# Kernel optimization log

Hardware: AMD Instinct MI355X
Metric: run time of the kernel (lower is better)

Reference implementation:

```python
import jax, jax.numpy as jnp
import numpy as np

NUM_HEADS = 8

def setup_inputs() -> dict:
    key = jax.random.key(0)
    ks = jax.random.split(key, 9)
    b, s, d = 2, 2048, 512
    e = d * NUM_HEADS  # 4096
    sc = 0.02
    return {
        "x": jax.random.normal(ks[0], (b, s, d), jnp.float32),
        "Wq": jax.random.normal(ks[1], (e, d), jnp.float32) * sc,
        "bq": jax.random.normal(ks[2], (e,), jnp.float32) * sc,
        "Wk": jax.random.normal(ks[3], (e, d), jnp.float32) * sc,
        "bk": jax.random.normal(ks[4], (e,), jnp.float32) * sc,
        "Wv": jax.random.normal(ks[5], (e, d), jnp.float32) * sc,
        "bv": jax.random.normal(ks[6], (e,), jnp.float32) * sc,
        "Wo": jax.random.normal(ks[7], (d, e), jnp.float32) * sc,
        "bo": jax.random.normal(ks[8], (d,), jnp.float32) * sc,
    }

def reference(x, Wq, bq, Wk, bk, Wv, bv, Wo, bo):
    b, s, d = x.shape
    h = NUM_HEADS
    hd = d  # head_dim == model_dimension in this module
    # QKV projections: [b, s, h*hd]
    q = (x @ Wq.T + bq).reshape(b, s, h, hd)
    k = (x @ Wk.T + bk).reshape(b, s, h, hd)
    v = (x @ Wv.T + bv).reshape(b, s, h, hd)
    # scores: [b, h, s_q, s_k]
    scores = jnp.einsum("bqhd,bkhd->bhqk", q, k) / jnp.sqrt(jnp.float32(hd))
    attn = jax.nn.softmax(scores, axis=-1)
    ctx = jnp.einsum("bhqk,bkhd->bqhd", attn, v).reshape(b, s, h * hd)
    return ctx @ Wo.T + bo
```

## Files before the change

kernel.cpp:

```cpp
#include <hip/hip_runtime.h>
#include <hip/hip_bf16.h>

typedef __hip_bfloat16 bf16t;
typedef short bf16x8 __attribute__((ext_vector_type(8)));
typedef float f32x4 __attribute__((ext_vector_type(4)));

__device__ __forceinline__ float b2f(short s) {
    unsigned u = ((unsigned)(unsigned short)s) << 16;
    float f;
    __builtin_memcpy(&f, &u, 4);
    return f;
}

__device__ __forceinline__ unsigned short f2b(float f) {
    unsigned u;
    __builtin_memcpy(&u, &f, 4);
    unsigned r = (u + 0x7fffu + ((u >> 16) & 1u)) >> 16;
    return (unsigned short)r;
}

__device__ __forceinline__ void gload_lds16(const void* g, void* l) {
    __builtin_amdgcn_global_load_lds(
        (const __attribute__((address_space(1))) void*)g,
        (__attribute__((address_space(3))) void*)l,
        16, 0, 0);
}

template<int EPI>
__global__ __launch_bounds__(512, 2)
void gemm8p(const bf16t* __restrict__ Ag, const bf16t* __restrict__ Bg,
            void* __restrict__ Cg, const float* __restrict__ bias,
            int K, int lda, int ldb, int ldc,
            long aOffB, long aOffH, long bOffB, long bOffH,
            long cOffB, long cOffH, float scale)
{
    __shared__ __align__(16) char lds8[131072];

    unsigned gx = gridDim.x, gy = gridDim.y;
    unsigned nwg = gx * gy * gridDim.z;
    unsigned wg = (blockIdx.z * gy + blockIdx.y) * gx + blockIdx.x;
    if ((nwg & 7u) == 0u) wg = (wg & 7u) * (nwg >> 3) + (wg >> 3);
    const unsigned pz = wg / (gx * gy);
    const unsigned prem = wg - pz * gx * gy;
    const unsigned py = prem / gx;
    const unsigned px = prem - py * gx;

    const int zb = pz >> 3, zh = pz & 7;
    const int brow = py * 256;
    const int bcol = px * 256;

    const size_t ldab = (size_t)lda * 2;
    const size_t ldbb = (size_t)ldb * 2;
    const char* Agb = (const char*)(Ag + (size_t)zb * aOffB + (size_t)zh * aOffH)
                      + (size_t)brow * ldab;
    const char* Bgb = (const char*)(Bg + (size_t)zb * bOffB + (size_t)zh * bOffH)
                      + (size_t)bcol * ldbb;

    const int t    = threadIdx.x;
    const int lane = t & 63;
    const int wid  = t >> 6;
    const int wm   = wid >> 2;
    const int wn   = wid & 3;
    const int lr   = lane & 15;
    const int lk   = lane >> 4;

    const int srow = t >> 2;
    const int scg  = (t & 3) ^ ((srow >> 1) & 3);
    const size_t aSrc = (size_t)srow * ldab + (size_t)scg * 16;
    const size_t bSrc = (size_t)srow * ldbb + (size_t)scg * 16;
    const int dst0 = t * 16;
    char* ldsA = lds8;
    char* ldsB = lds8 + 65536;

    const int rchunk = lk ^ ((lr >> 1) & 3);
    const int aByte = (wm * 128 + lr) * 64 + rchunk * 16;
    const int bByte = (wn * 64 + lr) * 64 + rchunk * 16;

    f32x4 acc[8][4];
#pragma unroll
    for (int i = 0; i < 8; ++i)
#pragma unroll
        for (int j = 0; j < 4; ++j)
            acc[i][j] = (f32x4){0.f, 0.f, 0.f, 0.f};

    const int nk = K >> 5;

#define STAGE_A(kt, bufi) do {                                              \
        const char* s_ = Agb + (size_t)(kt) * 64 + aSrc;                    \
        char* d_ = ldsA + (bufi) * 16384 + dst0;                            \
        gload_lds16(s_, d_);                                                \
        gload_lds16(s_ + 128 * ldab, d_ + 8192);                            \
    } while (0)
#define STAGE_B(kt, bufi) do {                                              \
        const char* s_ = Bgb + (size_t)(kt) * 64 + bSrc;                    \
        char* d_ = ldsB + (bufi) * 16384 + dst0;                            \
        gload_lds16(s_, d_);                                                \
        gload_lds16(s_ + 128 * ldbb, d_ + 8192);                            \
    } while (0)

    const int npro = nk < 3 ? nk : 3;
    for (int p = 0; p < npro; ++p) { STAGE_A(p, p & 3); STAGE_B(p, p & 3); }
    if (npro == 3) asm volatile("s_waitcnt vmcnt(8)" ::: "memory");
    else           asm volatile("s_waitcnt vmcnt(0)" ::: "memory");
    __builtin_amdgcn_s_barrier();

    for (int kt = 0; kt < nk; ++kt) {
        const int buf  = kt & 3;
        const int bufS = (kt + 3) & 3;
        const bool st  = (kt + 3) < nk;
        const char* lA = ldsA + buf * 16384;
        const char* lB = ldsB + buf * 16384;

        bf16x8 af[4], bfv[4];
#pragma unroll
        for (int i = 0; i < 4; ++i) af[i]  = *(const bf16x8*)(lA + aByte + i * 1024);
#pragma unroll
        for (int j = 0; j < 4; ++j) bfv[j] = *(const bf16x8*)(lB + bByte + j * 1024);
        if (st) STAGE_A(kt + 3, bufS);
        __builtin_amdgcn_s_barrier();
        asm volatile("s_waitcnt lgkmcnt(0)" ::: "memory");
        __builtin_amdgcn_s_setprio(1);
#pragma unroll
        for (int i = 0; i < 4; ++i)
#pragma unroll
            for (int j = 0; j < 4; ++j)
                acc[i][j] = __builtin_amdgcn_mfma_f32_16x16x32_bf16(af[i], bfv[j], acc[i][j], 0, 0, 0);
        __builtin_amdgcn_s_setprio(0);
        __builtin_amdgcn_s_barrier();

        bf16x8 af2[4];
#pragma unroll
        for (int i = 0; i < 4; ++i) af2[i] = *(const bf16x8*)(lA + aByte + (i + 4) * 1024);
        if (st) STAGE_B(kt + 3, bufS);
        if (st)                  asm volatile("s_waitcnt vmcnt(8)" ::: "memory");
        else if (kt + 2 < nk)    asm volatile("s_waitcnt vmcnt(4)" ::: "memory");
        else if (kt + 1 < nk)    asm volatile("s_waitcnt vmcnt(0)" ::: "memory");
        __builtin_amdgcn_s_barrier();
        asm volatile("s_waitcnt lgkmcnt(0)" ::: "memory");
        __builtin_amdgcn_s_setprio(1);
#pragma unroll
        for (int i = 0; i < 4; ++i)
#pragma unroll
            for (int j = 0; j < 4; ++j)
                acc[i + 4][j] = __builtin_amdgcn_mfma_f32_16x16x32_bf16(af2[i], bfv[j], acc[i + 4][j], 0, 0, 0);
        __builtin_amdgcn_s_setprio(0);
        __builtin_amdgcn_s_barrier();
    }
#undef STAGE_A
#undef STAGE_B

    if (EPI == 0) {
        __syncthreads();
        unsigned short* lC = (unsigned short*)lds8;
#pragma unroll
        for (int i = 0; i < 8; ++i)
#pragma unroll
            for (int j = 0; j < 4; ++j) {
                int col = wn * 64 + j * 16 + lr;
                float badd = bias ? bias[bcol + col] : 0.f;
#pragma unroll
                for (int r = 0; r < 4; ++r) {
                    int row = wm * 128 + i * 16 + lk * 4 + r;
                    lC[row * 256 + col] = f2b(acc[i][j][r] * scale + badd);
                }
            }
        __syncthreads();
        unsigned short* C = (unsigned short*)((bf16t*)Cg + (size_t)zb * cOffB + (size_t)zh * cOffH);
#pragma unroll
        for (int p = 0; p < 16; ++p) {
            int c  = p * 512 + t;
            int row = c >> 5;
            int cc  = c & 31;
            bf16x8 v = *(const bf16x8*)(lC + (size_t)c * 8);
            *(bf16x8*)(C + (size_t)(brow + row) * ldc + bcol + cc * 8) = v;
        }
    } else {
        unsigned short* C = (unsigned short*)Cg;
#pragma unroll
        for (int i = 0; i < 8; ++i)
#pragma unroll
            for (int j = 0; j < 4; ++j) {
                int col = bcol + wn * 64 + j * 16 + lr;
                int hh = col >> 9, dd = col & 511;
                float badd = bias ? bias[col] : 0.f;
                int row0 = brow + wm * 128 + i * 16 + lk * 4;
                int bb = row0 >> 11, ss0 = row0 & 2047;
                ushort4 pack;
                pack.x = f2b(acc[i][j][0] * scale + badd);
                pack.y = f2b(acc[i][j][1] * scale + badd);
                pack.z = f2b(acc[i][j][2] * scale + badd);
                pack.w = f2b(acc[i][j][3] * scale + badd);
                size_t addr = ((((size_t)(bb * 8 + hh)) * 512 + dd) << 11) + (size_t)ss0;
                *(ushort4*)(C + addr) = pack;
            }
    }
}

__global__ __launch_bounds__(256)
void gemm_of32(const bf16t* __restrict__ Ag, const bf16t* __restrict__ Bg,
               float* __restrict__ Cg, const float* __restrict__ bias,
               int K, int lda, int ldb, int ldc)
{
    __shared__ __align__(16) bf16t As[128 * 32];
    __shared__ __align__(16) bf16t Bs[64 * 32];

    unsigned gx = gridDim.x, gy = gridDim.y;
    unsigned nwg = gx * gy;
    unsigned wg = blockIdx.y * gx + blockIdx.x;
    if ((nwg & 7u) == 0u) wg = (wg & 7u) * (nwg >> 3) + (wg >> 3);
    const unsigned py = wg / gx;
    const unsigned px = wg - py * gx;
    const int brow = py * 128;
    const int bcol = px * 64;

    const int t    = threadIdx.x;
    const int lane = t & 63;
    const int wid  = t >> 6;
    const int wr   = wid >> 1, wc = wid & 1;
    const int lr   = lane & 15;
    const int lk   = lane >> 4;

    const size_t ldab = (size_t)lda * 2;
    const size_t ldbb = (size_t)ldb * 2;

    f32x4 acc[4][2];
#pragma unroll
    for (int i = 0; i < 4; ++i)
#pragma unroll
        for (int j = 0; j < 2; ++j)
            acc[i][j] = (f32x4){0.f, 0.f, 0.f, 0.f};

    const int srow = t >> 2;
    const int scg  = (t & 3) ^ ((srow >> 1) & 3);
    const char* Abase = (const char*)Ag + (size_t)brow * ldab;
    const char* Bbase = (const char*)Bg + (size_t)bcol * ldbb;
    const size_t aSrc = (size_t)srow * ldab + (size_t)scg * 16;
    const size_t bSrc = (size_t)srow * ldbb + (size_t)scg * 16;
    char* AsB = (char*)As;
    char* BsB = (char*)Bs;

    const int rchunk = lk ^ ((lr >> 1) & 3);
    const int aByte = (wr * 64 + lr) * 64 + rchunk * 16;
    const int bByte = (wc * 32 + lr) * 64 + rchunk * 16;

    const int nk = K >> 5;
    for (int kt = 0; kt < nk; ++kt) {
        const size_t kOff = (size_t)kt * 64;
        gload_lds16(Abase + aSrc + kOff,             AsB + t * 16);
        gload_lds16(Abase + aSrc + 64 * ldab + kOff, AsB + t * 16 + 4096);
        gload_lds16(Bbase + bSrc + kOff,             BsB + t * 16);
        asm volatile("s_waitcnt vmcnt(0)" ::: "memory");
        __syncthreads();

        bf16x8 af[4], bfv[2];
#pragma unroll
        for (int i = 0; i < 4; ++i)
            af[i] = *(const bf16x8*)(AsB + aByte + i * 1024);
#pragma unroll
        for (int j = 0; j < 2; ++j)
            bfv[j] = *(const bf16x8*)(BsB + bByte + j * 1024);
#pragma unroll
        for (int i = 0; i < 4; ++i)
#pragma unroll
            for (int j = 0; j < 2; ++j)
                acc[i][j] = __builtin_amdgcn_mfma_f32_16x16x32_bf16(af[i], bfv[j], acc[i][j], 0, 0, 0);
        __syncthreads();
    }

    const int orow = brow + wr * 64;
    const int ocol = bcol + wc * 32;
#pragma unroll
    for (int i = 0; i < 4; ++i)
#pragma unroll
        for (int j = 0; j < 2; ++j) {
            int col = ocol + j * 16 + lr;
            float badd = bias[col];
#pragma unroll
            for (int r = 0; r < 4; ++r) {
                int row = orow + i * 16 + lk * 4 + r;
                Cg[(size_t)row * ldc + col] = acc[i][j][r] + badd;
            }
        }
}

__global__ __launch_bounds__(256)
void softmax2048(bf16t* __restrict__ Sp)
{
    size_t row = blockIdx.x;
    bf16x8* p = (bf16x8*)(Sp + row * 2048);
    int t = threadIdx.x;
    bf16x8 raw = p[t];
    float v[8];
    float mx = -3.0e38f;
#pragma unroll
    for (int i = 0; i < 8; ++i) { v[i] = b2f(raw[i]); mx = fmaxf(mx, v[i]); }
#pragma unroll
    for (int off = 1; off < 64; off <<= 1) mx = fmaxf(mx, __shfl_xor(mx, off));
    __shared__ float redm[4], reds[4];
    int wid = t >> 6, lane = t & 63;
    if (lane == 0) redm[wid] = mx;
    __syncthreads();
    mx = fmaxf(fmaxf(redm[0], redm[1]), fmaxf(redm[2], redm[3]));
    float sum = 0.f;
#pragma unroll
    for (int i = 0; i < 8; ++i) { v[i] = __expf(v[i] - mx); sum += v[i]; }
#pragma unroll
    for (int off = 1; off < 64; off <<= 1) sum += __shfl_xor(sum, off);
    if (lane == 0) reds[wid] = sum;
    __syncthreads();
    sum = reds[0] + reds[1] + reds[2] + reds[3];
    float inv = 1.0f / sum;
    bf16x8 o;
#pragma unroll
    for (int i = 0; i < 8; ++i) o[i] = (short)f2b(v[i] * inv);
    p[t] = o;
}

__global__ __launch_bounds__(256)
void cvt5(const float* __restrict__ s0, const float* __restrict__ s1,
          const float* __restrict__ s2, const float* __restrict__ s3,
          const float* __restrict__ s4,
          bf16t* __restrict__ d0, bf16t* __restrict__ d1,
          bf16t* __restrict__ d2, bf16t* __restrict__ d3,
          bf16t* __restrict__ d4)
{
    const float* s;
    bf16t* d;
    switch (blockIdx.y) {
        case 0: s = s0; d = d0; break;
        case 1: s = s1; d = d1; break;
        case 2: s = s2; d = d2; break;
        case 3: s = s3; d = d3; break;
        default: s = s4; d = d4; break;
    }
    int i = blockIdx.x * 256 + threadIdx.x;
    float4 f = ((const float4*)s)[i];
    ushort4 o;
    o.x = f2b(f.x); o.y = f2b(f.y); o.z = f2b(f.z); o.w = f2b(f.w);
    ((ushort4*)d)[i] = o;
}

extern "C" void kernel_launch(void* const* d_in, const int* in_sizes, int n_in,
                              void* d_out, int out_size, void* d_ws, size_t ws_size,
                              hipStream_t stream)
{
    const float* x  = (const float*)d_in[0];
    const float* Wq = (const float*)d_in[1];
    const float* bq = (const float*)d_in[2];
    const float* Wk = (const float*)d_in[3];
    const float* bk = (const float*)d_in[4];
    const float* Wv = (const float*)d_in[5];
    const float* bv = (const float*)d_in[6];
    const float* Wo = (const float*)d_in[7];
    const float* bo = (const float*)d_in[8];

    const int Bn = 2, Sn = 2048, Dn = 512, Hn = 8, En = 4096;
    const int Mn = Bn * Sn;
    const float scl = 0.044194173824159216f;

    bf16t* base = (bf16t*)d_ws;
    size_t off = 0;
    bf16t* Qb  = base + off; off += (size_t)Mn * En;
    bf16t* Kb  = base + off; off += (size_t)Mn * En;
    bf16t* Vt  = base + off; off += (size_t)Mn * En;
    bf16t* Xb  = base + off; off += (size_t)Mn * Dn;
    bf16t* Wqb = base + off; off += (size_t)En * Dn;
    bf16t* Wkb = base + off; off += (size_t)En * Dn;
    bf16t* Wvb = base + off; off += (size_t)En * Dn;
    bf16t* Wob = base + off; off += (size_t)Dn * En;
    bf16t* Sb  = base + off;

    cvt5<<<dim3(2048, 5, 1), 256, 0, stream>>>(x, Wq, Wk, Wv, Wo,
                                               Xb, Wqb, Wkb, Wvb, Wob);

    gemm8p<0><<<dim3(En / 256, Mn / 256, 1), 512, 0, stream>>>(
        Xb, Wqb, Qb, bq, Dn, Dn, Dn, En, 0, 0, 0, 0, 0, 0, 1.0f);
    gemm8p<0><<<dim3(En / 256, Mn / 256, 1), 512, 0, stream>>>(
        Xb, Wkb, Kb, bk, Dn, Dn, Dn, En, 0, 0, 0, 0, 0, 0, 1.0f);
    gemm8p<2><<<dim3(En / 256, Mn / 256, 1), 512, 0, stream>>>(
        Xb, Wvb, Vt, bv, Dn, Dn, Dn, En, 0, 0, 0, 0, 0, 0, 1.0f);

    gemm8p<0><<<dim3(Sn / 256, Sn / 256, 16), 512, 0, stream>>>(
        Qb, Kb, Sb, nullptr, Dn, En, En, Sn,
        (long)Sn * En, (long)Dn, (long)Sn * En, (long)Dn,
        (long)Hn * Sn * Sn, (long)Sn * Sn, scl);

    softmax2048<<<Bn * Hn * Sn, 256, 0, stream>>>(Sb);

    gemm8p<0><<<dim3(Dn / 256, Sn / 256, 16), 512, 0, stream>>>(
        Sb, Vt, Qb, nullptr, Sn, Sn, Sn, En,
        (long)Hn * Sn * Sn, (long)Sn * Sn, (long)Hn * Dn * Sn, (long)Dn * Sn,
        (long)Sn * En, (long)Dn, 1.0f);

    gemm_of32<<<dim3(Dn / 64, Mn / 128, 1), 256, 0, stream>>>(
        Qb, Wob, (float*)d_out, bo, En, En, En, Dn);
}
```

Baseline: 358.1 us.

## Fuse softmax into QK and PV GEMM epilogues, pipeline output projection GEMM

Drops the standalone softmax pass. The QK^T GEMM epilogue now applies exp to the scaled scores with no max subtraction, writes unnormalized probabilities, and stores per-tile row partial sums to a workspace. The PV GEMM epilogue adds up those partials and multiplies by the reciprocal row sum. It also removes two barriers and their lgkmcnt waits in the gemm8p main loop, and turns gemm_of32 into a 4-buffer async-LDS pipeline. Skipping the max subtraction means exp can overflow for large logits, and the removed barriers could in principle race.

```diff
diff --git a/kernel.cpp b/kernel.cpp
--- a/kernel.cpp
+++ b/kernel.cpp
@@ -30,6 +30,7 @@
 __global__ __launch_bounds__(512, 2)
 void gemm8p(const bf16t* __restrict__ Ag, const bf16t* __restrict__ Bg,
             void* __restrict__ Cg, const float* __restrict__ bias,
+            float* __restrict__ part,
             int K, int lda, int ldb, int ldc,
             long aOffB, long aOffH, long bOffB, long bOffH,
             long cOffB, long cOffH, float scale)
@@ -117,8 +118,6 @@
 #pragma unroll
         for (int j = 0; j < 4; ++j) bfv[j] = *(const bf16x8*)(lB + bByte + j * 1024);
         if (st) STAGE_A(kt + 3, bufS);
-        __builtin_amdgcn_s_barrier();
-        asm volatile("s_waitcnt lgkmcnt(0)" ::: "memory");
         __builtin_amdgcn_s_setprio(1);
 #pragma unroll
         for (int i = 0; i < 4; ++i)
@@ -126,6 +125,7 @@
             for (int j = 0; j < 4; ++j)
                 acc[i][j] = __builtin_amdgcn_mfma_f32_16x16x32_bf16(af[i], bfv[j], acc[i][j], 0, 0, 0);
         __builtin_amdgcn_s_setprio(0);
+        asm volatile("" ::: "memory");
         __builtin_amdgcn_s_barrier();
 
         bf16x8 af2[4];
@@ -135,8 +135,6 @@
         if (st)                  asm volatile("s_waitcnt vmcnt(8)" ::: "memory");
         else if (kt + 2 < nk)    asm volatile("s_waitcnt vmcnt(4)" ::: "memory");
         else if (kt + 1 < nk)    asm volatile("s_waitcnt vmcnt(0)" ::: "memory");
-        __builtin_amdgcn_s_barrier();
-        asm volatile("s_waitcnt lgkmcnt(0)" ::: "memory");
         __builtin_amdgcn_s_setprio(1);
 #pragma unroll
         for (int i = 0; i < 4; ++i)
@@ -144,12 +142,97 @@
             for (int j = 0; j < 4; ++j)
                 acc[i + 4][j] = __builtin_amdgcn_mfma_f32_16x16x32_bf16(af2[i], bfv[j], acc[i + 4][j], 0, 0, 0);
         __builtin_amdgcn_s_setprio(0);
+        asm volatile("" ::: "memory");
         __builtin_amdgcn_s_barrier();
     }
 #undef STAGE_A
 #undef STAGE_B
 
-    if (EPI == 0) {
+    if (EPI == 4) {
+#pragma unroll
+        for (int i = 0; i < 8; ++i)
+#pragma unroll
+            for (int j = 0; j < 4; ++j)
+#pragma unroll
+                for (int r = 0; r < 4; ++r)
+                    acc[i][j][r] = __expf(acc[i][j][r] * scale);
+#pragma unroll
+        for (int i = 0; i < 8; ++i)
+#pragma unroll
+            for (int r = 0; r < 4; ++r) {
+                float v = acc[i][0][r] + acc[i][1][r] + acc[i][2][r] + acc[i][3][r];
+                v += __shfl_xor(v, 1);
+                v += __shfl_xor(v, 2);
+                v += __shfl_xor(v, 4);
+                v += __shfl_xor(v, 8);
+                if (lr == 0)
+                    part[((size_t)pz * 2048 + brow + wm * 128 + i * 16 + lk * 4 + r) * 32
+                         + px * 4 + wn] = v;
+            }
+        __syncthreads();
+        unsigned short* lC = (unsigned short*)lds8;
+#pragma unroll
+        for (int i = 0; i < 8; ++i)
+#pragma unroll
+            for (int j = 0; j < 4; ++j) {
+                int col = wn * 64 + j * 16 + lr;
+#pragma unroll
+                for (int r = 0; r < 4; ++r) {
+                    int row = wm * 128 + i * 16 + lk * 4 + r;
+                    lC[row * 256 + col] = f2b(acc[i][j][r]);
+                }
+            }
+        __syncthreads();
+        unsigned short* C = (unsigned short*)((bf16t*)Cg + (size_t)zb * cOffB + (size_t)zh * cOffH);
+#pragma unroll
+        for (int p = 0; p < 16; ++p) {
+            int c  = p * 512 + t;
+            int row = c >> 5;
+            int cc  = c & 31;
+            bf16x8 v = *(const bf16x8*)(lC + (size_t)c * 8);
+            *(bf16x8*)(C + (size_t)(brow + row) * ldc + bcol + cc * 8) = v;
+        }
+    } else if (EPI == 3) {
+        __syncthreads();
+        float* ldsInv = (float*)lds8;
+        if (t < 256) {
+            const float* pp = part + ((size_t)pz * 2048 + brow + t) * 32;
+            float s = 0.f;
+#pragma unroll
+            for (int p = 0; p < 32; ++p) s += pp[p];
+            ldsInv[t] = 1.0f / s;
+        }
+        __syncthreads();
+        float linv[8][4];
+#pragma unroll
+        for (int i = 0; i < 8; ++i)
+#pragma unroll
+            for (int r = 0; r < 4; ++r)
+                linv[i][r] = ldsInv[wm * 128 + i * 16 + lk * 4 + r];
+        __syncthreads();
+        unsigned short* lC = (unsigned short*)lds8;
+#pragma unroll
+        for (int i = 0; i < 8; ++i)
+#pragma unroll
+            for (int j = 0; j < 4; ++j) {
+                int col = wn * 64 + j * 16 + lr;
+#pragma unroll
+                for (int r = 0; r < 4; ++r) {
+                    int row = wm * 128 + i * 16 + lk * 4 + r;
+                    lC[row * 256 + col] = f2b(acc[i][j][r] * linv[i][r]);
+                }
+            }
+        __syncthreads();
+        unsigned short* C = (unsigned short*)((bf16t*)Cg + (size_t)zb * cOffB + (size_t)zh * cOffH);
+#pragma unroll
+        for (int p = 0; p < 16; ++p) {
+            int c  = p * 512 + t;
+            int row = c >> 5;
+            int cc  = c & 31;
+            bf16x8 v = *(const bf16x8*)(lC + (size_t)c * 8);
+            *(bf16x8*)(C + (size_t)(brow + row) * ldc + bcol + cc * 8) = v;
+        }
+    } else if (EPI == 0) {
         __syncthreads();
         unsigned short* lC = (unsigned short*)lds8;
 #pragma unroll
@@ -196,13 +279,12 @@
     }
 }
 
-__global__ __launch_bounds__(256)
+__global__ __launch_bounds__(256, 3)
 void gemm_of32(const bf16t* __restrict__ Ag, const bf16t* __restrict__ Bg,
                float* __restrict__ Cg, const float* __restrict__ bias,
                int K, int lda, int ldb, int ldc)
 {
-    __shared__ __align__(16) bf16t As[128 * 32];
-    __shared__ __align__(16) bf16t Bs[64 * 32];
+    __shared__ __align__(16) char lds[49152];
 
     unsigned gx = gridDim.x, gy = gridDim.y;
     unsigned nwg = gx * gy;
@@ -222,50 +304,67 @@
 
     const size_t ldab = (size_t)lda * 2;
     const size_t ldbb = (size_t)ldb * 2;
-
-    f32x4 acc[4][2];
-#pragma unroll
-    for (int i = 0; i < 4; ++i)
-#pragma unroll
-        for (int j = 0; j < 2; ++j)
-            acc[i][j] = (f32x4){0.f, 0.f, 0.f, 0.f};
+    const char* Agb = (const char*)Ag + (size_t)brow * ldab;
+    const char* Bgb = (const char*)Bg + (size_t)bcol * ldbb;
 
     const int srow = t >> 2;
     const int scg  = (t & 3) ^ ((srow >> 1) & 3);
-    const char* Abase = (const char*)Ag + (size_t)brow * ldab;
-    const char* Bbase = (const char*)Bg + (size_t)bcol * ldbb;
     const size_t aSrc = (size_t)srow * ldab + (size_t)scg * 16;
     const size_t bSrc = (size_t)srow * ldbb + (size_t)scg * 16;
-    char* AsB = (char*)As;
-    char* BsB = (char*)Bs;
+    char* ldsA = lds;
+    char* ldsB = lds + 32768;
 
     const int rchunk = lk ^ ((lr >> 1) & 3);
     const int aByte = (wr * 64 + lr) * 64 + rchunk * 16;
     const int bByte = (wc * 32 + lr) * 64 + rchunk * 16;
 
+    f32x4 acc[4][2];
+#pragma unroll
+    for (int i = 0; i < 4; ++i)
+#pragma unroll
+        for (int j = 0; j < 2; ++j)
+            acc[i][j] = (f32x4){0.f, 0.f, 0.f, 0.f};
+
     const int nk = K >> 5;
+
+#define STAGE_O(kt, bufi) do {                                              \
+        const char* sa_ = Agb + (size_t)(kt) * 64 + aSrc;                   \
+        gload_lds16(sa_,             ldsA + (bufi) * 8192 + t * 16);        \
+        gload_lds16(sa_ + 64 * ldab, ldsA + (bufi) * 8192 + 4096 + t * 16); \
+        gload_lds16(Bgb + (size_t)(kt) * 64 + bSrc,                         \
+                    ldsB + (bufi) * 4096 + t * 16);                         \
+    } while (0)
+
+    for (int p = 0; p < 3; ++p) STAGE_O(p, p);
+    asm volatile("s_waitcnt vmcnt(6)" ::: "memory");
+    __builtin_amdgcn_s_barrier();
+
     for (int kt = 0; kt < nk; ++kt) {
-        const size_t kOff = (size_t)kt * 64;
-        gload_lds16(Abase + aSrc + kOff,             AsB + t * 16);
-        gload_lds16(Abase + aSrc + 64 * ldab + kOff, AsB + t * 16 + 4096);
-        gload_lds16(Bbase + bSrc + kOff,             BsB + t * 16);
-        asm volatile("s_waitcnt vmcnt(0)" ::: "memory");
-        __syncthreads();
+        const int buf  = kt & 3;
+        const bool st  = (kt + 3) < nk;
+        const char* lA = ldsA + buf * 8192;
+        const char* lB = ldsB + buf * 4096;
 
         bf16x8 af[4], bfv[2];
 #pragma unroll
-        for (int i = 0; i < 4; ++i)
-            af[i] = *(const bf16x8*)(AsB + aByte + i * 1024);
-#pragma unroll
-        for (int j = 0; j < 2; ++j)
-            bfv[j] = *(const bf16x8*)(BsB + bByte + j * 1024);
+        for (int i = 0; i < 4; ++i) af[i]  = *(const bf16x8*)(lA + aByte + i * 1024);
+#pragma unroll
+        for (int j = 0; j < 2; ++j) bfv[j] = *(const bf16x8*)(lB + bByte + j * 1024);
+        if (st) STAGE_O(kt + 3, (kt + 3) & 3);
+        if (st)                  asm volatile("s_waitcnt vmcnt(6)" ::: "memory");
+        else if (kt + 2 < nk)    asm volatile("s_waitcnt vmcnt(3)" ::: "memory");
+        else if (kt + 1 < nk)    asm volatile("s_waitcnt vmcnt(0)" ::: "memory");
+        __builtin_amdgcn_s_setprio(1);
 #pragma unroll
         for (int i = 0; i < 4; ++i)
 #pragma unroll
             for (int j = 0; j < 2; ++j)
                 acc[i][j] = __builtin_amdgcn_mfma_f32_16x16x32_bf16(af[i], bfv[j], acc[i][j], 0, 0, 0);
-        __syncthreads();
+        __builtin_amdgcn_s_setprio(0);
+        asm volatile("" ::: "memory");
+        __builtin_amdgcn_s_barrier();
     }
+#undef STAGE_O
 
     const int orow = brow + wr * 64;
     const int ocol = bcol + wc * 32;
@@ -281,39 +380,6 @@
                 Cg[(size_t)row * ldc + col] = acc[i][j][r] + badd;
             }
         }
-}
-
-__global__ __launch_bounds__(256)
-void softmax2048(bf16t* __restrict__ Sp)
-{
-    size_t row = blockIdx.x;
-    bf16x8* p = (bf16x8*)(Sp + row * 2048);
-    int t = threadIdx.x;
-    bf16x8 raw = p[t];
-    float v[8];
-    float mx = -3.0e38f;
-#pragma unroll
-    for (int i = 0; i < 8; ++i) { v[i] = b2f(raw[i]); mx = fmaxf(mx, v[i]); }
-#pragma unroll
-    for (int off = 1; off < 64; off <<= 1) mx = fmaxf(mx, __shfl_xor(mx, off));
-    __shared__ float redm[4], reds[4];
-    int wid = t >> 6, lane = t & 63;
-    if (lane == 0) redm[wid] = mx;
-    __syncthreads();
-    mx = fmaxf(fmaxf(redm[0], redm[1]), fmaxf(redm[2], redm[3]));
-    float sum = 0.f;
-#pragma unroll
-    for (int i = 0; i < 8; ++i) { v[i] = __expf(v[i] - mx); sum += v[i]; }
-#pragma unroll
-    for (int off = 1; off < 64; off <<= 1) sum += __shfl_xor(sum, off);
-    if (lane == 0) reds[wid] = sum;
-    __syncthreads();
-    sum = reds[0] + reds[1] + reds[2] + reds[3];
-    float inv = 1.0f / sum;
-    bf16x8 o;
-#pragma unroll
-    for (int i = 0; i < 8; ++i) o[i] = (short)f2b(v[i] * inv);
-    p[t] = o;
 }
 
 __global__ __launch_bounds__(256)
@@ -368,27 +434,26 @@
     bf16t* Wkb = base + off; off += (size_t)En * Dn;
     bf16t* Wvb = base + off; off += (size_t)En * Dn;
     bf16t* Wob = base + off; off += (size_t)Dn * En;
+    float* Pt  = (float*)(base + off); off += (size_t)16 * Sn * 32 * 2;
     bf16t* Sb  = base + off;
 
     cvt5<<<dim3(2048, 5, 1), 256, 0, stream>>>(x, Wq, Wk, Wv, Wo,
                                                Xb, Wqb, Wkb, Wvb, Wob);
 
     gemm8p<0><<<dim3(En / 256, Mn / 256, 1), 512, 0, stream>>>(
-        Xb, Wqb, Qb, bq, Dn, Dn, Dn, En, 0, 0, 0, 0, 0, 0, 1.0f);
+        Xb, Wqb, Qb, bq, nullptr, Dn, Dn, Dn, En, 0, 0, 0, 0, 0, 0, 1.0f);
     gemm8p<0><<<dim3(En / 256, Mn / 256, 1), 512, 0, stream>>>(
-        Xb, Wkb, Kb, bk, Dn, Dn, Dn, En, 0, 0, 0, 0, 0, 0, 1.0f);
+        Xb, Wkb, Kb, bk, nullptr, Dn, Dn, Dn, En, 0, 0, 0, 0, 0, 0, 1.0f);
     gemm8p<2><<<dim3(En / 256, Mn / 256, 1), 512, 0, stream>>>(
-        Xb, Wvb, Vt, bv, Dn, Dn, Dn, En, 0, 0, 0, 0, 0, 0, 1.0f);
-
-    gemm8p<0><<<dim3(Sn / 256, Sn / 256, 16), 512, 0, stream>>>(
-        Qb, Kb, Sb, nullptr, Dn, En, En, Sn,
+        Xb, Wvb, Vt, bv, nullptr, Dn, Dn, Dn, En, 0, 0, 0, 0, 0, 0, 1.0f);
+
+    gemm8p<4><<<dim3(Sn / 256, Sn / 256, 16), 512, 0, stream>>>(
+        Qb, Kb, Sb, nullptr, Pt, Dn, En, En, Sn,
         (long)Sn * En, (long)Dn, (long)Sn * En, (long)Dn,
         (long)Hn * Sn * Sn, (long)Sn * Sn, scl);
 
-    softmax2048<<<Bn * Hn * Sn, 256, 0, stream>>>(Sb);
-
-    gemm8p<0><<<dim3(Dn / 256, Sn / 256, 16), 512, 0, stream>>>(
-        Sb, Vt, Qb, nullptr, Sn, Sn, Sn, En,
+    gemm8p<3><<<dim3(Dn / 256, Sn / 256, 16), 512, 0, stream>>>(
+        Sb, Vt, Qb, nullptr, Pt, Sn, Sn, Sn, En,
         (long)Hn * Sn * Sn, (long)Sn * Sn, (long)Hn * Dn * Sn, (long)Dn * Sn,
         (long)Sn * En, (long)Dn, 1.0f);
 
```

After: 300.0 us. -16.2%, faster.
